# Performance work log

Measured on AMD Instinct MI355X. Metric: run time of the kernel, lower is better.

The kernel has to match this reference:

```python
import jax, jax.numpy as jnp
import numpy as np

NOT_EPSILON = 1.0
W_SCALE = 0.05  # scaled randn init for numerical stability of swishmax logits

H, T, A, C = 8, 1024, 64, 256  # heads, key/query size, attention size, compress size


def swishmax(x, axis):
    m = jnp.max(x, axis=axis, keepdims=True)
    xe = x * jnp.exp(x - m)
    return xe / (jnp.sum(jnp.abs(xe), axis=axis, keepdims=True) + NOT_EPSILON)


def setup_inputs() -> dict:
    key = jax.random.key(0)
    ks = jax.random.split(key, 7)
    B, Q, K = 2, 2048, 2048
    return {
        "query_tokens": jax.random.normal(ks[0], (B, Q, T), dtype=jnp.float32),
        "key_tokens": jax.random.normal(ks[1], (B, K, T), dtype=jnp.float32),
        "key_down": jax.random.normal(ks[2], (H, T, A), dtype=jnp.float32) * W_SCALE,
        "query_down": jax.random.normal(ks[3], (H, T, A), dtype=jnp.float32) * W_SCALE,
        "query_down_bias": jax.random.normal(ks[4], (H, 1, A), dtype=jnp.float32) * W_SCALE,
        "value_down": jax.random.normal(ks[5], (H, T, C), dtype=jnp.float32) * W_SCALE,
        "value_up": jax.random.normal(ks[6], (H, C, T), dtype=jnp.float32) * W_SCALE,
    }


def reference(query_tokens, key_tokens, key_down, query_down, query_down_bias, value_down, value_up):
    # key/query projections: [B,K,T] x [H,T,A] -> [B,H,K,A]
    k = jnp.einsum('bkt,hta->bhka', key_tokens, key_down)
    q = jnp.einsum('bqt,hta->bhqa', query_tokens, query_down) + query_down_bias[None]  # [B,H,Q,A]
    # attention logits: key @ query^T -> [B,H,K,Q]
    logits = jnp.einsum('bhka,bhqa->bhkq', k, q)
    attn = swishmax(logits, axis=-2)  # normalized over keys (dim=-2)
    # sum_k key_tokens[b,k,:] * attn[b,h,k,q]  ==  [B,H,Q,T] (matmul form of the outer-product sum)
    vs = jnp.einsum('bhkq,bkt->bhqt', attn, key_tokens)
    # compress path: value_down then value_up
    vs = jnp.einsum('bhqc,hct->bhqt', jnp.einsum('bhqt,htc->bhqc', vs, value_down), value_up)
    return vs.sum(axis=1)  # sum over heads -> [B,Q,T]
```

## Files before the change

### kernel.cpp

```cpp
#include <hip/hip_runtime.h>
#include <hip/hip_fp16.h>
#include <math.h>


typedef _Float16 f16;
typedef _Float16 f16x4 __attribute__((ext_vector_type(4)));
typedef _Float16 f16x8 __attribute__((ext_vector_type(8)));
typedef short s16x4 __attribute__((ext_vector_type(4)));
typedef short bf16x8 __attribute__((ext_vector_type(8)));
typedef float f32x4 __attribute__((ext_vector_type(4)));

#define MFMA_F16(a, b, c) __builtin_amdgcn_mfma_f32_16x16x32_f16(a, b, c, 0, 0, 0)
#define MFMA_BF16(a, b, c) __builtin_amdgcn_mfma_f32_16x16x32_bf16(a, b, c, 0, 0, 0)

__device__ __forceinline__ void g2lds16(const void* g, void* l) {
  __builtin_amdgcn_global_load_lds((__attribute__((address_space(1))) void*)g,
                                   (__attribute__((address_space(3))) void*)l, 16, 0, 0);
}

__device__ __forceinline__ short f32_bf16(float x) {
  union { float f; unsigned u; } v; v.f = x;
  unsigned r = v.u + 0x7FFFu + ((v.u >> 16) & 1u);
  return (short)(r >> 16);
}
__device__ __forceinline__ float bf16_f32(short h) {
  union { unsigned u; float f; } v; v.u = ((unsigned)(unsigned short)h) << 16;
  return v.f;
}

__global__ __launch_bounds__(256) void ew_split2(const float* __restrict__ qin,
                                                 const float* __restrict__ kin,
                                                 short* __restrict__ qhi,
                                                 short* __restrict__ qlo,
                                                 short* __restrict__ khi,
                                                 short* __restrict__ klo,
                                                 f16* __restrict__ kf) {
  int i = blockIdx.x * 256 + threadIdx.x;
  const bool isK = i >= 1048576;
  const int j = isK ? i - 1048576 : i;
  const float* in = isK ? kin : qin;
  f32x4 v = ((const f32x4*)in)[j];
  s16x4 h, l;
  f16x4 f;
#pragma unroll
  for (int e = 0; e < 4; e++) {
    short he = f32_bf16(v[e]);
    h[e] = he;
    l[e] = f32_bf16(v[e] - bf16_f32(he));
    f[e] = (f16)v[e];
  }
  if (isK) {
    ((s16x4*)khi)[j] = h;
    ((s16x4*)klo)[j] = l;
    ((f16x4*)kf)[j] = f;
  } else {
    ((s16x4*)qhi)[j] = h;
    ((s16x4*)qlo)[j] = l;
  }
}

__global__ __launch_bounds__(256) void transpose_all(
    const float* __restrict__ qdw, const float* __restrict__ kdw,
    const float* __restrict__ vdw, const float* __restrict__ vup,
    short* __restrict__ wqT_hi, short* __restrict__ wqT_lo,
    short* __restrict__ wkT_hi, short* __restrict__ wkT_lo,
    f16* __restrict__ vdT, f16* __restrict__ vuT) {
  __shared__ float t[64][65];
  int idx = blockIdx.x;
  const float* in;
  short *bhi = nullptr, *blo = nullptr;
  f16* fo = nullptr;
  int R, C, cb, rb;
  size_t batch;
  if (idx < 256) {
    bool isQ = idx < 128;
    int i = isQ ? idx : idx - 128;
    in = isQ ? qdw : kdw;
    bhi = isQ ? wqT_hi : wkT_hi;
    blo = isQ ? wqT_lo : wkT_lo;
    R = 1024; C = 64; cb = 0; rb = (i & 15) * 64;
    batch = (size_t)(i >> 4) * R * C;
  } else if (idx < 768) {
    int i = idx - 256;
    in = vdw; fo = vdT;
    R = 1024; C = 256; cb = (i & 3) * 64; rb = ((i >> 2) & 15) * 64;
    batch = (size_t)(i >> 6) * R * C;
  } else {
    int i = idx - 768;
    in = vup; fo = vuT;
    R = 2048; C = 1024; cb = (i & 15) * 64; rb = (i >> 4) * 64;
    batch = 0;
  }
  int tid = threadIdx.x;
#pragma unroll
  for (int i = 0; i < 4; i++) {
    int r = (tid >> 4) + i * 16, c4 = (tid & 15) * 4;
    f32x4 v = *(const f32x4*)(in + batch + (size_t)(rb + r) * C + cb + c4);
    t[r][c4] = v[0]; t[r][c4 + 1] = v[1]; t[r][c4 + 2] = v[2]; t[r][c4 + 3] = v[3];
  }
  __syncthreads();
#pragma unroll
  for (int i = 0; i < 4; i++) {
    int c = (tid >> 4) + i * 16, r4 = (tid & 15) * 4;
    float v0 = t[r4][c], v1 = t[r4 + 1][c], v2 = t[r4 + 2][c], v3 = t[r4 + 3][c];
    size_t o = batch + (size_t)(cb + c) * R + rb + r4;
    if (bhi) {
      s16x4 h = {f32_bf16(v0), f32_bf16(v1), f32_bf16(v2), f32_bf16(v3)};
      *(s16x4*)(bhi + o) = h;
      s16x4 l = {f32_bf16(v0 - bf16_f32(h[0])), f32_bf16(v1 - bf16_f32(h[1])),
                 f32_bf16(v2 - bf16_f32(h[2])), f32_bf16(v3 - bf16_f32(h[3]))};
      *(s16x4*)(blo + o) = l;
    }
    if (fo) {
      f16x4 fv = {(f16)v0, (f16)v1, (f16)v2, (f16)v3};
      *(f16x4*)(fo + o) = fv;
    }
  }
}

__global__ __launch_bounds__(256, 2) void proj_gemm(
    const short* __restrict__ qtok_hi, const short* __restrict__ qtok_lo,
    const short* __restrict__ ktok_hi, const short* __restrict__ ktok_lo,
    const short* __restrict__ wqT_hi, const short* __restrict__ wqT_lo,
    const short* __restrict__ wkT_hi, const short* __restrict__ wkT_lo,
    const float* __restrict__ bias, short* __restrict__ q_split,
    short* __restrict__ k_split) {
  const bool isQ = (blockIdx.z == 0);
  const short* Ahi = isQ ? qtok_hi : ktok_hi;
  const short* Alo = isQ ? qtok_lo : ktok_lo;
  const short* Bhi = isQ ? wqT_hi : wkT_hi;
  const short* Blo = isQ ? wqT_lo : wkT_lo;
  short* outp = isQ ? q_split : k_split;

  __shared__ __attribute__((aligned(16))) short sm[2][12288];

  int tid = threadIdx.x, w = tid >> 6, lane = tid & 63, g = lane >> 4, li = lane & 15;
  int mb = blockIdx.y * 64, nb = blockIdx.x * 128;
  int wm = (w >> 1) * 32, wn = (w & 1) * 64;

  f32x4 acc[2][4] = {};

  auto STAGE = [&](int kb, int buf) {
    {
      int off = tid * 16;
      int row = off >> 6, ss = ((off >> 4) & 3) ^ ((row >> 1) & 3);
      size_t src = (size_t)(mb + row) * 1024 + kb + ss * 8;
      g2lds16(Ahi + src, (char*)&sm[buf][0] + w * 1024);
      g2lds16(Alo + src, (char*)&sm[buf][2048] + w * 1024);
    }
#pragma unroll
    for (int i = 0; i < 2; i++) {
      int off = i * 4096 + tid * 16;
      int row = off >> 6, ss = ((off >> 4) & 3) ^ ((row >> 1) & 3);
      size_t src = (size_t)(nb + row) * 1024 + kb + ss * 8;
      g2lds16(Bhi + src, (char*)&sm[buf][4096] + i * 4096 + w * 1024);
      g2lds16(Blo + src, (char*)&sm[buf][8192] + i * 4096 + w * 1024);
    }
  };

  STAGE(0, 0);
  __syncthreads();
  for (int kb = 0; kb < 1024; kb += 32) {
    int cur = (kb >> 5) & 1;
    if (kb + 32 < 1024) STAGE(kb + 32, cur ^ 1);
    bf16x8 af[2][2], bf[4][2];
#pragma unroll
    for (int f = 0; f < 2; f++) {
      int ra = wm + f * 16 + li, sa = g ^ ((ra >> 1) & 3);
      af[f][0] = *(const bf16x8*)&sm[cur][ra * 32 + sa * 8];
      af[f][1] = *(const bf16x8*)&sm[cur][2048 + ra * 32 + sa * 8];
    }
#pragma unroll
    for (int f = 0; f < 4; f++) {
      int rb = wn + f * 16 + li, sb = g ^ ((rb >> 1) & 3);
      bf[f][0] = *(const bf16x8*)&sm[cur][4096 + rb * 32 + sb * 8];
      bf[f][1] = *(const bf16x8*)&sm[cur][8192 + rb * 32 + sb * 8];
    }
#pragma unroll
    for (int mf = 0; mf < 2; mf++)
#pragma unroll
      for (int nf = 0; nf < 4; nf++) {
        acc[mf][nf] = MFMA_BF16(af[mf][0], bf[nf][0], acc[mf][nf]);
        acc[mf][nf] = MFMA_BF16(af[mf][0], bf[nf][1], acc[mf][nf]);
        acc[mf][nf] = MFMA_BF16(af[mf][1], bf[nf][0], acc[mf][nf]);
      }
    __syncthreads();
  }
#pragma unroll
  for (int mf = 0; mf < 2; mf++)
#pragma unroll
    for (int nf = 0; nf < 4; nf++)
#pragma unroll
      for (int r = 0; r < 4; r++) {
        int m = mb + wm + mf * 16 + 4 * g + r;
        int n = nb + wn + nf * 16 + li;
        float v = acc[mf][nf][r];
        if (isQ) v += bias[n];
        short hi = f32_bf16(v);
        short lo = f32_bf16(v - bf16_f32(hi));
        size_t base = ((size_t)((m >> 11) * 8 + (n >> 6)) * 2048 + (m & 2047)) * 128;
        outp[base + (n & 63)] = hi;
        outp[base + 64 + (n & 63)] = lo;
      }
}

__global__ __launch_bounds__(256, 4) void kv_gemm(const f16* __restrict__ A,
                                                  const f16* __restrict__ Bm,
                                                  f16* __restrict__ kvT) {
  __shared__ __attribute__((aligned(16))) f16 sm[2][6144];
  int tid = threadIdx.x, w = tid >> 6, lane = tid & 63, g = lane >> 4, li = lane & 15;
  int mb = blockIdx.y * 64, nb = blockIdx.x * 128;
  int wm = (w >> 1) * 32, wn = (w & 1) * 64;
  f32x4 acc[2][4] = {};

  auto STAGE = [&](int kb, int buf) {
    {
      int off = tid * 16;
      int row = off >> 6, ss = ((off >> 4) & 3) ^ ((row >> 1) & 3);
      g2lds16(A + (size_t)(mb + row) * 1024 + kb + ss * 8, (char*)&sm[buf][0] + w * 1024);
    }
#pragma unroll
    for (int i = 0; i < 2; i++) {
      int off = i * 4096 + tid * 16;
      int row = off >> 6, ss = ((off >> 4) & 3) ^ ((row >> 1) & 3);
      g2lds16(Bm + (size_t)(nb + row) * 1024 + kb + ss * 8,
              (char*)&sm[buf][2048] + i * 4096 + w * 1024);
    }
  };

  STAGE(0, 0);
  __syncthreads();
  for (int kb = 0; kb < 1024; kb += 32) {
    int cur = (kb >> 5) & 1;
    if (kb + 32 < 1024) STAGE(kb + 32, cur ^ 1);
    f16x8 af[2], bf[4];
#pragma unroll
    for (int f = 0; f < 2; f++) {
      int ra = wm + f * 16 + li, sa = g ^ ((ra >> 1) & 3);
      af[f] = *(const f16x8*)&sm[cur][ra * 32 + sa * 8];
    }
#pragma unroll
    for (int f = 0; f < 4; f++) {
      int rb = wn + f * 16 + li, sb = g ^ ((rb >> 1) & 3);
      bf[f] = *(const f16x8*)&sm[cur][2048 + rb * 32 + sb * 8];
    }
#pragma unroll
    for (int mf = 0; mf < 2; mf++)
#pragma unroll
      for (int nf = 0; nf < 4; nf++)
        acc[mf][nf] = MFMA_F16(af[mf], bf[nf], acc[mf][nf]);
    __syncthreads();
  }
#pragma unroll
  for (int mf = 0; mf < 2; mf++)
#pragma unroll
    for (int nf = 0; nf < 4; nf++) {
      int m = mb + wm + mf * 16 + 4 * g;
      int n = nb + wn + nf * 16 + li;
      f16x4 v = {(f16)acc[mf][nf][0], (f16)acc[mf][nf][1], (f16)acc[mf][nf][2],
                 (f16)acc[mf][nf][3]};
      int bh = (m >> 11) * 8 + (n >> 8);
      size_t o = (size_t)bh * 524288 + (size_t)((m & 2047) >> 5) * 8192 +
                 (size_t)(n & 255) * 32 + (m & 31);
      *(f16x4*)(kvT + o) = v;
    }
}

__global__ __launch_bounds__(256, 2) void flash_attn(const short* __restrict__ q_split,
                                                     const short* __restrict__ k_split,
                                                     const f16* __restrict__ kvT,
                                                     f16* __restrict__ vs_c) {
  __shared__ __attribute__((aligned(16))) short k_lds[2][8192];
  __shared__ __attribute__((aligned(16))) f16 p_lds[2][4096];
  __shared__ float sc_lds[2][4][16];
  __shared__ float fix_lds[64];

  const int bid = blockIdx.x;
  const int bh = ((bid & 7) << 1) + ((bid >> 3) & 1);
  const int qb = bid >> 4;
  const int tid = threadIdx.x;
  const int w = tid >> 6, lane = tid & 63, g = lane >> 4, li = lane & 15;

  const short* qrow = q_split + ((size_t)bh * 2048 + qb * 64 + w * 16 + li) * 128;
  bf16x8 qf[2][2];
#pragma unroll
  for (int ach = 0; ach < 2; ach++)
#pragma unroll
    for (int hl = 0; hl < 2; hl++)
      qf[ach][hl] = *(const bf16x8*)(qrow + hl * 64 + ach * 32 + g * 8);

  const short* kbase = k_split + (size_t)bh * 262144;
  const f16* kvbase = kvT + (size_t)bh * 524288 + (size_t)w * 64 * 32 + li * 32 + g * 8;

  float m_cur = -INFINITY, m_true = -INFINITY, l_run = 0.f;
  f32x4 acc[4][4] = {};
  f16x8 kvf[2][4];

  auto STAGE_K = [&](int t, int buf) {
#pragma unroll
    for (int i = 0; i < 4; i++) {
      int off = (w * 4 + i) * 1024 + lane * 16;
      int row = off >> 8;
      int ss = ((off >> 4) & 15) ^ (row & 7);
      g2lds16(kbase + t * 8192 + row * 128 + ss * 8,
              (char*)k_lds[buf] + (w * 4 + i) * 1024);
    }
  };

  auto LOADKV = [&](int t) {
#pragma unroll
    for (int h = 0; h < 2; h++) {
      const f16* p = kvbase + (size_t)(2 * t + h) * 8192;
#pragma unroll
      for (int ct = 0; ct < 4; ct++) kvf[h][ct] = *(const f16x8*)(p + ct * 512);
    }
  };

  auto QKSM = [&](int buf) {
    f32x4 s[4] = {};
    __builtin_amdgcn_s_setprio(1);
#pragma unroll
    for (int kc = 0; kc < 4; kc++) {
      const int r = kc * 16 + li;
#pragma unroll
      for (int ach = 0; ach < 2; ach++) {
        int sh = (ach * 4 + g) ^ (r & 7);
        int sl = (8 + ach * 4 + g) ^ (r & 7);
        bf16x8 khi = *(const bf16x8*)((const char*)k_lds[buf] + r * 256 + sh * 16);
        bf16x8 klo = *(const bf16x8*)((const char*)k_lds[buf] + r * 256 + sl * 16);
        s[kc] = MFMA_BF16(khi, qf[ach][0], s[kc]);
        s[kc] = MFMA_BF16(khi, qf[ach][1], s[kc]);
        s[kc] = MFMA_BF16(klo, qf[ach][0], s[kc]);
      }
    }
    __builtin_amdgcn_s_setprio(0);

    float tmax = -INFINITY;
#pragma unroll
    for (int kc = 0; kc < 4; kc++)
      tmax = fmaxf(tmax, fmaxf(fmaxf(s[kc][0], s[kc][1]), fmaxf(s[kc][2], s[kc][3])));
    tmax = fmaxf(tmax, __shfl_xor(tmax, 16));
    tmax = fmaxf(tmax, __shfl_xor(tmax, 32));
    m_true = fmaxf(m_true, tmax);
    float sc = 1.0f;
    if (__any(tmax > m_cur + 4.0f)) {
      float mn = fmaxf(m_cur, tmax);
      sc = __expf(m_cur - mn);
      l_run *= sc;
      m_cur = mn;
    }
    if (g == 0) sc_lds[buf][w][li] = sc;

    float ls = 0.f;
    float pv[16];
#pragma unroll
    for (int kc = 0; kc < 4; kc++)
#pragma unroll
      for (int r2 = 0; r2 < 4; r2++) {
        float sv = s[kc][r2];
        float e = sv * __expf(sv - m_cur);
        pv[kc * 4 + r2] = e;
        ls += fabsf(e);
      }
    ls += __shfl_xor(ls, 16);
    ls += __shfl_xor(ls, 32);
    l_run += ls;

#pragma unroll
    for (int kc = 0; kc < 4; kc++) {
      f16x4 p4 = {(f16)pv[kc * 4], (f16)pv[kc * 4 + 1], (f16)pv[kc * 4 + 2],
                  (f16)pv[kc * 4 + 3]};
      int wb = ((w * 16 + li) * 128 + kc * 32 + g * 8) ^ ((li & 7) << 4);
      *(f16x4*)((char*)p_lds[buf] + wb) = p4;
    }
  };

  STAGE_K(0, 0);
  STAGE_K(1, 1);
  __syncthreads();
  QKSM(0);

#pragma unroll 2
  for (int t = 0; t < 32; t++) {
    const int cur = t & 1;
    __syncthreads();
    LOADKV(t);
    if (t < 30) STAGE_K(t + 2, cur);
    if (t < 31) QKSM(cur ^ 1);

#pragma unroll
    for (int qt = 0; qt < 4; qt++) {
      float scq = sc_lds[cur][qt][li];
      if (__any(scq != 1.0f)) {
#pragma unroll
        for (int ct = 0; ct < 4; ct++) acc[ct][qt] *= scq;
      }
    }

    __builtin_amdgcn_s_setprio(1);
#pragma unroll
    for (int qt = 0; qt < 4; qt++) {
#pragma unroll
      for (int h = 0; h < 2; h++) {
        int rb = ((qt * 16 + li) * 128 + h * 64 + g * 16) ^ ((li & 7) << 4);
        f16x8 pf = *(const f16x8*)((const char*)p_lds[cur] + rb);
#pragma unroll
        for (int ct = 0; ct < 4; ct++)
          acc[ct][qt] = MFMA_F16(kvf[h][ct], pf, acc[ct][qt]);
      }
    }
    __builtin_amdgcn_s_setprio(0);
  }

  float sfix = __expf(m_cur - m_true);
  float invd = sfix / (l_run * sfix + 1.0f);
  __syncthreads();
  if (g == 0) fix_lds[w * 16 + li] = invd;
  __syncthreads();
#pragma unroll
  for (int qt = 0; qt < 4; qt++) {
    float iv = fix_lds[qt * 16 + li];
    f16* orow = vs_c + ((size_t)(bh >> 3) * 2048 + qb * 64 + qt * 16 + li) * 2048 +
                (bh & 7) * 256 + w * 64 + g * 4;
#pragma unroll
    for (int ct = 0; ct < 4; ct++) {
      f16x4 v = {(f16)(acc[ct][qt][0] * iv), (f16)(acc[ct][qt][1] * iv),
                 (f16)(acc[ct][qt][2] * iv), (f16)(acc[ct][qt][3] * iv)};
      *(f16x4*)(orow + ct * 16) = v;
    }
  }
}

__global__ __launch_bounds__(256, 2) void final_gemm(const f16* __restrict__ A,
                                                     const f16* __restrict__ Bm,
                                                     float* __restrict__ outp) {
  __shared__ __attribute__((aligned(16))) f16 sm[2][6144];
  int tid = threadIdx.x, w = tid >> 6, lane = tid & 63, g = lane >> 4, li = lane & 15;
  int mb = blockIdx.y * 64, nb = blockIdx.x * 128;
  int wm = (w >> 1) * 32, wn = (w & 1) * 64;
  f32x4 acc[2][4] = {};

  auto STAGE = [&](int kb, int buf) {
    {
      int off = tid * 16;
      int row = off >> 6, ss = ((off >> 4) & 3) ^ ((row >> 1) & 3);
      g2lds16(A + (size_t)(mb + row) * 2048 + kb + ss * 8, (char*)&sm[buf][0] + w * 1024);
    }
#pragma unroll
    for (int i = 0; i < 2; i++) {
      int off = i * 4096 + tid * 16;
      int row = off >> 6, ss = ((off >> 4) & 3) ^ ((row >> 1) & 3);
      g2lds16(Bm + (size_t)(nb + row) * 2048 + kb + ss * 8,
              (char*)&sm[buf][2048] + i * 4096 + w * 1024);
    }
  };

  STAGE(0, 0);
  __syncthreads();
  for (int kb = 0; kb < 2048; kb += 32) {
    int cur = (kb >> 5) & 1;
    if (kb + 32 < 2048) STAGE(kb + 32, cur ^ 1);
    f16x8 af[2], bf[4];
#pragma unroll
    for (int f = 0; f < 2; f++) {
      int ra = wm + f * 16 + li, sa = g ^ ((ra >> 1) & 3);
      af[f] = *(const f16x8*)&sm[cur][ra * 32 + sa * 8];
    }
#pragma unroll
    for (int f = 0; f < 4; f++) {
      int rb = wn + f * 16 + li, sb = g ^ ((rb >> 1) & 3);
      bf[f] = *(const f16x8*)&sm[cur][2048 + rb * 32 + sb * 8];
    }
#pragma unroll
    for (int mf = 0; mf < 2; mf++)
#pragma unroll
      for (int nf = 0; nf < 4; nf++)
        acc[mf][nf] = MFMA_F16(af[mf], bf[nf], acc[mf][nf]);
    __syncthreads();
  }
#pragma unroll
  for (int mf = 0; mf < 2; mf++)
#pragma unroll
    for (int nf = 0; nf < 4; nf++)
#pragma unroll
      for (int r = 0; r < 4; r++) {
        int m = mb + wm + mf * 16 + 4 * g + r;
        int n = nb + wn + nf * 16 + li;
        outp[(size_t)m * 1024 + n] = acc[mf][nf][r];
      }
}

extern "C" void kernel_launch(void* const* d_in, const int* in_sizes, int n_in,
                              void* d_out, int out_size, void* d_ws, size_t ws_size,
                              hipStream_t stream) {
  (void)in_sizes; (void)n_in; (void)out_size; (void)ws_size;
  const float* qtok = (const float*)d_in[0];
  const float* ktok = (const float*)d_in[1];
  const float* kdw = (const float*)d_in[2];
  const float* qdw = (const float*)d_in[3];
  const float* qdb = (const float*)d_in[4];
  const float* vdw = (const float*)d_in[5];
  const float* vup = (const float*)d_in[6];

  char* ws = (char*)d_ws;
  size_t off = 0;
  auto take = [&](size_t n) { void* p = ws + off; off += (n + 255) & ~(size_t)255; return p; };

  short* qtok_hi = (short*)take(8u << 20);
  short* qtok_lo = (short*)take(8u << 20);
  short* ktok_hi = (short*)take(8u << 20);
  short* ktok_lo = (short*)take(8u << 20);
  f16* ktok_f = (f16*)take(8u << 20);
  short* wqT_hi = (short*)take(1u << 20);
  short* wqT_lo = (short*)take(1u << 20);
  short* wkT_hi = (short*)take(1u << 20);
  short* wkT_lo = (short*)take(1u << 20);
  f16* vdT = (f16*)take(4u << 20);
  f16* vuT = (f16*)take(4u << 20);
  short* q_split = (short*)take(8u << 20);
  short* k_split = (short*)take(8u << 20);
  f16* kvT = (f16*)(void*)ktok_hi;
  f16* vs_c = (f16*)(void*)qtok_hi;

  ew_split2<<<8192, 256, 0, stream>>>(qtok, ktok, qtok_hi, qtok_lo, ktok_hi,
                                      ktok_lo, ktok_f);
  transpose_all<<<1280, 256, 0, stream>>>(qdw, kdw, vdw, vup, wqT_hi, wqT_lo,
                                          wkT_hi, wkT_lo, vdT, vuT);
  proj_gemm<<<dim3(4, 64, 2), 256, 0, stream>>>(qtok_hi, qtok_lo, ktok_hi, ktok_lo,
                                                wqT_hi, wqT_lo, wkT_hi, wkT_lo, qdb,
                                                q_split, k_split);
  kv_gemm<<<dim3(16, 64), 256, 0, stream>>>(ktok_f, vdT, kvT);
  flash_attn<<<512, 256, 0, stream>>>(q_split, k_split, kvT, vs_c);
  final_gemm<<<dim3(8, 64), 256, 0, stream>>>(vs_c, vuT, (float*)d_out);
}
```

Before: 203.3 us.

## Split QK work across waves by key rows, drop K LDS staging

The flash attention kernel now has each wave load its own 16 key rows straight from global memory into registers and compute logits against all 64 queries, instead of staging K tiles through LDS. Column max and abs-sum are reduced across waves through small LDS arrays, so every wave keeps the full per-query running max and sum. The loop is re-pipelined: QK for tile t+1 overlaps PV for tile t-1, with a lighter lgkmcnt+barrier sync. This removes LDS traffic and the K staging, at the cost of more registers for four Q fragment sets and extra cross-wave reductions.

```diff
diff --git a/kernel.cpp b/kernel.cpp
--- a/kernel.cpp
+++ b/kernel.cpp
@@ -270,10 +270,9 @@
                                                      const short* __restrict__ k_split,
                                                      const f16* __restrict__ kvT,
                                                      f16* __restrict__ vs_c) {
-  __shared__ __attribute__((aligned(16))) short k_lds[2][8192];
   __shared__ __attribute__((aligned(16))) f16 p_lds[2][4096];
-  __shared__ float sc_lds[2][4][16];
-  __shared__ float fix_lds[64];
+  __shared__ __attribute__((aligned(16))) float pmax_lds[2][64][4];
+  __shared__ __attribute__((aligned(16))) float ls_lds[2][64][4];
 
   const int bid = blockIdx.x;
   const int bh = ((bid & 7) << 1) + ((bid >> 3) & 1);
@@ -281,32 +280,37 @@
   const int tid = threadIdx.x;
   const int w = tid >> 6, lane = tid & 63, g = lane >> 4, li = lane & 15;
 
-  const short* qrow = q_split + ((size_t)bh * 2048 + qb * 64 + w * 16 + li) * 128;
-  bf16x8 qf[2][2];
-#pragma unroll
-  for (int ach = 0; ach < 2; ach++)
-#pragma unroll
-    for (int hl = 0; hl < 2; hl++)
-      qf[ach][hl] = *(const bf16x8*)(qrow + hl * 64 + ach * 32 + g * 8);
-
-  const short* kbase = k_split + (size_t)bh * 262144;
-  const f16* kvbase = kvT + (size_t)bh * 524288 + (size_t)w * 64 * 32 + li * 32 + g * 8;
-
-  float m_cur = -INFINITY, m_true = -INFINITY, l_run = 0.f;
+  bf16x8 qf[4][2][2];
+#pragma unroll
+  for (int qt = 0; qt < 4; qt++) {
+    const short* qrow = q_split + ((size_t)bh * 2048 + qb * 64 + qt * 16 + li) * 128;
+#pragma unroll
+    for (int ach = 0; ach < 2; ach++)
+#pragma unroll
+      for (int hl = 0; hl < 2; hl++)
+        qf[qt][ach][hl] = *(const bf16x8*)(qrow + hl * 64 + ach * 32 + g * 8);
+  }
+
+  const short* kb = k_split + (size_t)bh * 262144 + (w * 16 + li) * 128 + g * 8;
+  const f16* kvbase = kvT + (size_t)bh * 524288 + (size_t)w * 2048 + li * 32 + g * 8;
+
   f32x4 acc[4][4] = {};
+  f32x4 s[4];
+  bf16x8 kf[2][2];
   f16x8 kvf[2][4];
-
-  auto STAGE_K = [&](int t, int buf) {
-#pragma unroll
-    for (int i = 0; i < 4; i++) {
-      int off = (w * 4 + i) * 1024 + lane * 16;
-      int row = off >> 8;
-      int ss = ((off >> 4) & 15) ^ (row & 7);
-      g2lds16(kbase + t * 8192 + row * 128 + ss * 8,
-              (char*)k_lds[buf] + (w * 4 + i) * 1024);
-    }
-  };
-
+  float m_cur[4], m_true[4], l_run[4], sc_[4];
+#pragma unroll
+  for (int qt = 0; qt < 4; qt++) {
+    m_cur[qt] = -INFINITY; m_true[qt] = -INFINITY; l_run[qt] = 0.f; sc_[qt] = 1.f;
+  }
+
+  auto LOADK = [&](int t) {
+#pragma unroll
+    for (int ach = 0; ach < 2; ach++)
+#pragma unroll
+      for (int hl = 0; hl < 2; hl++)
+        kf[ach][hl] = *(const bf16x8*)(kb + t * 8192 + hl * 64 + ach * 32);
+  };
   auto LOADKV = [&](int t) {
 #pragma unroll
     for (int h = 0; h < 2; h++) {
@@ -316,110 +320,115 @@
     }
   };
 
-  auto QKSM = [&](int buf) {
-    f32x4 s[4] = {};
+  auto QK = [&](int par) {
+#pragma unroll
+    for (int qt = 0; qt < 4; qt++) s[qt] = (f32x4){0.f, 0.f, 0.f, 0.f};
     __builtin_amdgcn_s_setprio(1);
 #pragma unroll
-    for (int kc = 0; kc < 4; kc++) {
-      const int r = kc * 16 + li;
+    for (int qt = 0; qt < 4; qt++)
 #pragma unroll
       for (int ach = 0; ach < 2; ach++) {
-        int sh = (ach * 4 + g) ^ (r & 7);
-        int sl = (8 + ach * 4 + g) ^ (r & 7);
-        bf16x8 khi = *(const bf16x8*)((const char*)k_lds[buf] + r * 256 + sh * 16);
-        bf16x8 klo = *(const bf16x8*)((const char*)k_lds[buf] + r * 256 + sl * 16);
-        s[kc] = MFMA_BF16(khi, qf[ach][0], s[kc]);
-        s[kc] = MFMA_BF16(khi, qf[ach][1], s[kc]);
-        s[kc] = MFMA_BF16(klo, qf[ach][0], s[kc]);
-      }
-    }
+        s[qt] = MFMA_BF16(kf[ach][0], qf[qt][ach][0], s[qt]);
+        s[qt] = MFMA_BF16(kf[ach][0], qf[qt][ach][1], s[qt]);
+        s[qt] = MFMA_BF16(kf[ach][1], qf[qt][ach][0], s[qt]);
+      }
     __builtin_amdgcn_s_setprio(0);
-
-    float tmax = -INFINITY;
-#pragma unroll
-    for (int kc = 0; kc < 4; kc++)
-      tmax = fmaxf(tmax, fmaxf(fmaxf(s[kc][0], s[kc][1]), fmaxf(s[kc][2], s[kc][3])));
-    tmax = fmaxf(tmax, __shfl_xor(tmax, 16));
-    tmax = fmaxf(tmax, __shfl_xor(tmax, 32));
-    m_true = fmaxf(m_true, tmax);
-    float sc = 1.0f;
-    if (__any(tmax > m_cur + 4.0f)) {
-      float mn = fmaxf(m_cur, tmax);
-      sc = __expf(m_cur - mn);
-      l_run *= sc;
-      m_cur = mn;
-    }
-    if (g == 0) sc_lds[buf][w][li] = sc;
-
-    float ls = 0.f;
-    float pv[16];
-#pragma unroll
-    for (int kc = 0; kc < 4; kc++)
-#pragma unroll
-      for (int r2 = 0; r2 < 4; r2++) {
-        float sv = s[kc][r2];
-        float e = sv * __expf(sv - m_cur);
-        pv[kc * 4 + r2] = e;
-        ls += fabsf(e);
-      }
-    ls += __shfl_xor(ls, 16);
-    ls += __shfl_xor(ls, 32);
-    l_run += ls;
-
-#pragma unroll
-    for (int kc = 0; kc < 4; kc++) {
-      f16x4 p4 = {(f16)pv[kc * 4], (f16)pv[kc * 4 + 1], (f16)pv[kc * 4 + 2],
-                  (f16)pv[kc * 4 + 3]};
-      int wb = ((w * 16 + li) * 128 + kc * 32 + g * 8) ^ ((li & 7) << 4);
-      *(f16x4*)((char*)p_lds[buf] + wb) = p4;
-    }
-  };
-
-  STAGE_K(0, 0);
-  STAGE_K(1, 1);
-  __syncthreads();
-  QKSM(0);
+#pragma unroll
+    for (int qt = 0; qt < 4; qt++) {
+      float tm = fmaxf(fmaxf(s[qt][0], s[qt][1]), fmaxf(s[qt][2], s[qt][3]));
+      tm = fmaxf(tm, __shfl_xor(tm, 16));
+      tm = fmaxf(tm, __shfl_xor(tm, 32));
+      if (lane < 16) pmax_lds[par][qt * 16 + lane][w] = tm;
+    }
+  };
+
+  auto BPHASE = [&](int t) {
+    const int par = t & 1;
+    if (t > 0) {
+      const int pl = (t - 1) & 1;
+#pragma unroll
+      for (int qt = 0; qt < 4; qt++) {
+        f32x4 l4 = *(const f32x4*)ls_lds[pl][qt * 16 + li];
+        l_run[qt] += (l4[0] + l4[1]) + (l4[2] + l4[3]);
+      }
+    }
+#pragma unroll
+    for (int qt = 0; qt < 4; qt++) {
+      f32x4 m4 = *(const f32x4*)pmax_lds[par][qt * 16 + li];
+      float tmax = fmaxf(fmaxf(m4[0], m4[1]), fmaxf(m4[2], m4[3]));
+      m_true[qt] = fmaxf(m_true[qt], tmax);
+      sc_[qt] = 1.0f;
+      if (__any(tmax > m_cur[qt] + 4.0f)) {
+        float mn = fmaxf(m_cur[qt], tmax);
+        sc_[qt] = __expf(m_cur[qt] - mn);
+        l_run[qt] *= sc_[qt];
+        m_cur[qt] = mn;
+      }
+      float lsum = 0.f;
+      f16x4 p4;
+#pragma unroll
+      for (int r = 0; r < 4; r++) {
+        float sv = s[qt][r];
+        float e = sv * __expf(sv - m_cur[qt]);
+        p4[r] = (f16)e;
+        lsum += fabsf(e);
+      }
+      int wb = ((qt * 16 + li) * 128 + w * 32 + g * 8) ^ ((li & 7) << 4);
+      *(f16x4*)((char*)p_lds[par] + wb) = p4;
+      lsum += __shfl_xor(lsum, 16);
+      lsum += __shfl_xor(lsum, 32);
+      if (lane < 16) ls_lds[par][qt * 16 + lane][w] = lsum;
+    }
+  };
+
+  auto PV = [&](int t) {
+    const int par = t & 1;
+    __builtin_amdgcn_s_setprio(1);
+#pragma unroll
+    for (int qt = 0; qt < 4; qt++)
+#pragma unroll
+      for (int h = 0; h < 2; h++) {
+        int rb = ((qt * 16 + li) * 128 + h * 64 + g * 16) ^ ((li & 7) << 4);
+        f16x8 pf = *(const f16x8*)((const char*)p_lds[par] + rb);
+#pragma unroll
+        for (int ct = 0; ct < 4; ct++)
+          acc[ct][qt] = MFMA_F16(kvf[h][ct], pf, acc[ct][qt]);
+      }
+    __builtin_amdgcn_s_setprio(0);
+  };
+
+  LOADK(0);
+  QK(0);
 
 #pragma unroll 2
   for (int t = 0; t < 32; t++) {
-    const int cur = t & 1;
-    __syncthreads();
-    LOADKV(t);
-    if (t < 30) STAGE_K(t + 2, cur);
-    if (t < 31) QKSM(cur ^ 1);
-
-#pragma unroll
-    for (int qt = 0; qt < 4; qt++) {
-      float scq = sc_lds[cur][qt][li];
-      if (__any(scq != 1.0f)) {
-#pragma unroll
-        for (int ct = 0; ct < 4; ct++) acc[ct][qt] *= scq;
-      }
-    }
-
-    __builtin_amdgcn_s_setprio(1);
-#pragma unroll
-    for (int qt = 0; qt < 4; qt++) {
-#pragma unroll
-      for (int h = 0; h < 2; h++) {
-        int rb = ((qt * 16 + li) * 128 + h * 64 + g * 16) ^ ((li & 7) << 4);
-        f16x8 pf = *(const f16x8*)((const char*)p_lds[cur] + rb);
-#pragma unroll
-        for (int ct = 0; ct < 4; ct++)
-          acc[ct][qt] = MFMA_F16(kvf[h][ct], pf, acc[ct][qt]);
-      }
-    }
-    __builtin_amdgcn_s_setprio(0);
-  }
-
-  float sfix = __expf(m_cur - m_true);
-  float invd = sfix / (l_run * sfix + 1.0f);
-  __syncthreads();
-  if (g == 0) fix_lds[w * 16 + li] = invd;
-  __syncthreads();
+    asm volatile("s_waitcnt lgkmcnt(0)\n\ts_barrier" ::: "memory");
+    if (t < 31) LOADK(t + 1);
+    if (t > 0) LOADKV(t - 1);
+    BPHASE(t);
+    if (t < 31) QK((t + 1) & 1);
+    if (t > 0) PV(t - 1);
+    if (__any(sc_[0] != 1.f || sc_[1] != 1.f || sc_[2] != 1.f || sc_[3] != 1.f)) {
+#pragma unroll
+      for (int qt = 0; qt < 4; qt++)
+#pragma unroll
+        for (int ct = 0; ct < 4; ct++) acc[ct][qt] *= sc_[qt];
+    }
+  }
+
+  asm volatile("s_waitcnt lgkmcnt(0)\n\ts_barrier" ::: "memory");
 #pragma unroll
   for (int qt = 0; qt < 4; qt++) {
-    float iv = fix_lds[qt * 16 + li];
+    f32x4 l4 = *(const f32x4*)ls_lds[1][qt * 16 + li];
+    l_run[qt] += (l4[0] + l4[1]) + (l4[2] + l4[3]);
+  }
+  LOADKV(31);
+  PV(31);
+
+#pragma unroll
+  for (int qt = 0; qt < 4; qt++) {
+    float sfix = __expf(m_cur[qt] - m_true[qt]);
+    float iv = sfix / (l_run[qt] * sfix + 1.0f);
     f16* orow = vs_c + ((size_t)(bh >> 3) * 2048 + qb * 64 + qt * 16 + li) * 2048 +
                 (bh & 7) * 256 + w * 64 + g * 4;
 #pragma unroll
```

Measured after the change: 216.8 us. +6.6%, slower.
